# Kernel optimization log

Hardware: AMD Instinct MI355X
Metric: run time of the kernel (lower is better)

The kernel has to match this reference:

```python
import jax, jax.numpy as jnp
import numpy as np

D_MODEL, D_STATE, D_CONV, EXPAND, DEPTH = 128, 16, 4, 2, 4
D_INNER = EXPAND * D_MODEL            # 256
DT_RANK = (D_MODEL + 15) // 16        # 8
C_IN, B, L = 3, 8, 8192


def _layernorm(x, w, b):
    mu = jnp.mean(x, axis=-1, keepdims=True)
    var = jnp.mean((x - mu) ** 2, axis=-1, keepdims=True)
    return (x - mu) * jax.lax.rsqrt(var + 1e-5) * w + b


def _mamba(x, in_w, conv_w, conv_b, xproj_w, dt_w, dt_b, A_log, Dp, out_w):
    # x: [B, L, d_model]
    Bb, Ll, _ = x.shape
    xz = x @ in_w.T                                  # [B,L,2*d_inner]
    u, z = jnp.split(xz, 2, axis=-1)
    # causal depthwise conv1d, kernel D_CONV
    xp = jnp.pad(u, ((0, 0), (D_CONV - 1, 0), (0, 0)))
    conv = conv_b + sum(xp[:, k:k + Ll, :] * conv_w[:, k] for k in range(D_CONV))
    u = jax.nn.silu(conv)                            # [B,L,d_inner]
    dbl = u @ xproj_w.T                              # [B,L,dt_rank+2*d_state]
    dt, Bm, Cm = jnp.split(dbl, [DT_RANK, DT_RANK + D_STATE], axis=-1)
    dt = jax.nn.softplus(dt @ dt_w.T + dt_b)         # [B,L,d_inner]
    A = -jnp.exp(A_log)                              # [d_inner,d_state]

    def step(h, inp):
        dt_t, B_t, C_t, u_t = inp                    # [B,d_inner],[B,d_state],[B,d_state],[B,d_inner]
        dA = jnp.exp(dt_t[..., None] * A)            # [B,d_inner,d_state]
        h = h * dA + (dt_t * u_t)[..., None] * B_t[:, None, :]
        y = jnp.einsum('bds,bs->bd', h, C_t)
        return h, y

    h0 = jnp.zeros((Bb, D_INNER, D_STATE), x.dtype)
    xs = (dt.transpose(1, 0, 2), Bm.transpose(1, 0, 2),
          Cm.transpose(1, 0, 2), u.transpose(1, 0, 2))
    _, ys = jax.lax.scan(step, h0, xs)               # ys: [L,B,d_inner]
    y = ys.transpose(1, 0, 2) + u * Dp
    y = y * jax.nn.silu(z)
    return y @ out_w.T                               # [B,L,d_model]


def setup_inputs() -> dict:
    key = jax.random.key(0)
    ks = jax.random.split(key, 12)
    s = lambda k, shape, scale: jax.random.normal(k, shape, jnp.float32) * scale
    inp = {
        'x': jax.random.normal(ks[0], (B, C_IN, L), jnp.float32),
        'proj_w': s(ks[1], (D_MODEL, C_IN), 0.5),
        'proj_b': jnp.zeros((D_MODEL,), jnp.float32),
        'ln_w': jnp.ones((DEPTH, D_MODEL), jnp.float32),
        'ln_b': jnp.zeros((DEPTH, D_MODEL), jnp.float32),
        'in_w': s(ks[2], (DEPTH, 2 * D_INNER, D_MODEL), D_MODEL ** -0.5),
        'conv_w': s(ks[3], (DEPTH, D_INNER, D_CONV), D_CONV ** -0.5),
        'conv_b': jnp.zeros((DEPTH, D_INNER), jnp.float32),
        'xproj_w': s(ks[4], (DEPTH, DT_RANK + 2 * D_STATE, D_INNER), D_INNER ** -0.5),
        'dt_w': s(ks[5], (DEPTH, D_INNER, DT_RANK), DT_RANK ** -0.5),
        'dt_b': jnp.full((DEPTH, D_INNER), -4.6, jnp.float32),  # softplus ~ small dt
        'A_log': jnp.broadcast_to(jnp.log(jnp.arange(1, D_STATE + 1, dtype=jnp.float32)),
                                  (DEPTH, D_INNER, D_STATE)).copy(),
        'Dp': jnp.ones((DEPTH, D_INNER), jnp.float32),
        'out_w': s(ks[6], (DEPTH, D_MODEL, D_INNER), D_INNER ** -0.5),
        'lnout_w': jnp.ones((D_MODEL,), jnp.float32),
        'lnout_b': jnp.zeros((D_MODEL,), jnp.float32),
    }
    return inp


def reference(x, proj_w, proj_b, ln_w, ln_b, in_w, conv_w, conv_b, xproj_w,
              dt_w, dt_b, A_log, Dp, out_w, lnout_w, lnout_b):
    # proj_in: Conv1d kernel_size=1 == pointwise linear over channels
    h = jnp.einsum('bcl,dc->bld', x, proj_w) + proj_b   # [B,L,d_model]
    for i in range(DEPTH):
        h = h + _mamba(_layernorm(h, ln_w[i], ln_b[i]),
                       in_w[i], conv_w[i], conv_b[i], xproj_w[i],
                       dt_w[i], dt_b[i], A_log[i], Dp[i], out_w[i])
    h = _layernorm(h, lnout_w, lnout_b)
    h_global = h.mean(axis=1)
    return h, h_global
```

## Files before the change

### kernel.cpp

```cpp
#include <hip/hip_runtime.h>
#include <hip/hip_bf16.h>
#include <math.h>

#define Bz     8
#define Lz     8192
#define DM     128
#define DI     256
#define DS     16
#define DTR    8
#define NDBL   40
#define DEPTHN 4
#define BLz    (Bz*Lz)
#define CHT    64
#define NCH    (Lz/CHT)
#define PADI   264
#define PADD   44

typedef unsigned short bf16_t;
typedef __attribute__((ext_vector_type(8))) __bf16 bf8;
typedef __attribute__((ext_vector_type(4))) float f4;
typedef __attribute__((ext_vector_type(8))) unsigned short us8;

__device__ __forceinline__ float bf2f(bf16_t u) {
    return __uint_as_float(((unsigned)u) << 16);
}
__device__ __forceinline__ bf16_t f2bf(float f) {
    unsigned u = __float_as_uint(f);
    u = u + 0x7FFFu + ((u >> 16) & 1u);
    return (bf16_t)(u >> 16);
}
__device__ __forceinline__ float fast_rcp(float x) {
    return __builtin_amdgcn_rcpf(x);
}

__device__ __forceinline__ void pow_tree(float e1, float dA[DS]) {
    float e2 = e1 * e1, e3 = e2 * e1, e4 = e2 * e2;
    float e8 = e4 * e4;
    dA[0] = e1;       dA[1] = e2;       dA[2] = e3;       dA[3] = e4;
    dA[4] = e4 * e1;  dA[5] = e4 * e2;  dA[6] = e4 * e3;  dA[7] = e8;
    dA[8] = e8 * e1;  dA[9] = e8 * e2;  dA[10] = e8 * e3; dA[11] = e8 * e4;
    dA[12] = e8 * dA[4]; dA[13] = e8 * dA[5]; dA[14] = e8 * dA[6];
    dA[15] = e8 * e8;
}

__global__ __launch_bounds__(256) void k_wconv(const float* __restrict__ inw,
                                               const float* __restrict__ ow,
                                               const float* __restrict__ xw,
                                               bf16_t* __restrict__ inwb,
                                               bf16_t* __restrict__ owb,
                                               bf16_t* __restrict__ xwb,
                                               float* __restrict__ hg) {
    int i = blockIdx.x * 256 + threadIdx.x;
    if (i < Bz * DM) hg[i] = 0.f;
    if (i < DEPTHN * 512 * DM) inwb[i] = f2bf(inw[i]);
    if (i < DEPTHN * DM * DI)  owb[i]  = f2bf(ow[i]);
    if (i < DEPTHN * 64 * DI) {
        int layer = i >> 14, rk = i & 16383, r = rk >> 8, k = rk & 255;
        xwb[i] = (r < NDBL) ? f2bf(xw[((size_t)layer * NDBL + r) * DI + k]) : (bf16_t)0;
    }
}

__global__ __launch_bounds__(256) void k_inproj(const float* __restrict__ x,
                                                const float* __restrict__ pw,
                                                const float* __restrict__ pb,
                                                float* __restrict__ h) {
    int t = blockIdx.x * 2 + (threadIdx.x >> 7);
    int d = threadIdx.x & 127;
    int b = t >> 13, l = t & (Lz - 1);
    float acc = pb[d];
#pragma unroll
    for (int c = 0; c < 3; ++c)
        acc += x[(size_t)(b * 3 + c) * Lz + l] * pw[d * 3 + c];
    h[(size_t)t * DM + d] = acc;
}

__global__ __launch_bounds__(256) void k_lnin(const float* __restrict__ h,
                                              const float* __restrict__ lw,
                                              const float* __restrict__ lb,
                                              const bf16_t* __restrict__ inwb,
                                              bf16_t* __restrict__ u_pre,
                                              bf16_t* __restrict__ zs) {
    __shared__ bf16_t sm[64 * PADI];
    bf16_t* xs = sm;
    int tid = threadIdx.x;
    int mBase = blockIdx.x * 64;

#pragma unroll
    for (int p = 0; p < 4; ++p) {
        int row = p * 16 + (tid >> 4);
        int lane = tid & 15;
        const float4* hp = (const float4*)(h + (size_t)(mBase + row) * DM + lane * 8);
        float4 v0 = hp[0], v1 = hp[1];
        float s = v0.x + v0.y + v0.z + v0.w + v1.x + v1.y + v1.z + v1.w;
        float q = v0.x*v0.x + v0.y*v0.y + v0.z*v0.z + v0.w*v0.w +
                  v1.x*v1.x + v1.y*v1.y + v1.z*v1.z + v1.w*v1.w;
#pragma unroll
        for (int off = 1; off < 16; off <<= 1) {
            s += __shfl_xor(s, off);
            q += __shfl_xor(q, off);
        }
        float mean = s * (1.f / DM);
        float var  = q * (1.f / DM) - mean * mean;
        float rstd = rsqrtf(var + 1e-5f);
        const float4* wp = (const float4*)(lw + lane * 8);
        const float4* bp = (const float4*)(lb + lane * 8);
        float4 w0 = wp[0], w1 = wp[1], b0 = bp[0], b1 = bp[1];
        ushort4 o0, o1;
        o0.x = f2bf((v0.x - mean) * rstd * w0.x + b0.x);
        o0.y = f2bf((v0.y - mean) * rstd * w0.y + b0.y);
        o0.z = f2bf((v0.z - mean) * rstd * w0.z + b0.z);
        o0.w = f2bf((v0.w - mean) * rstd * w0.w + b0.w);
        o1.x = f2bf((v1.x - mean) * rstd * w1.x + b1.x);
        o1.y = f2bf((v1.y - mean) * rstd * w1.y + b1.y);
        o1.z = f2bf((v1.z - mean) * rstd * w1.z + b1.z);
        o1.w = f2bf((v1.w - mean) * rstd * w1.w + b1.w);
        *(ushort4*)&xs[row * 136 + lane * 8]     = o0;
        *(ushort4*)&xs[row * 136 + lane * 8 + 4] = o1;
    }
    __syncthreads();

    int wave = tid >> 6, lane = tid & 63;
    int lr = lane & 15, lq = lane >> 4;
    int wn = wave * 128;
    f4 zf = {0.f, 0.f, 0.f, 0.f};
    f4 acc[4][8];
#pragma unroll
    for (int mi = 0; mi < 4; ++mi)
#pragma unroll
        for (int ni = 0; ni < 8; ++ni) acc[mi][ni] = zf;
    const bf16_t* Bp = inwb + (size_t)(wn + lr) * DM + lq * 8;
#pragma unroll
    for (int kk = 0; kk < DM; kk += 32) {
        bf8 af[4], bq[8];
#pragma unroll
        for (int mi = 0; mi < 4; ++mi)
            af[mi] = *(const bf8*)&xs[(mi * 16 + lr) * 136 + lq * 8 + kk];
#pragma unroll
        for (int ni = 0; ni < 8; ++ni)
            bq[ni] = *(const bf8*)(Bp + (size_t)ni * 16 * DM + kk);
#pragma unroll
        for (int mi = 0; mi < 4; ++mi)
#pragma unroll
            for (int ni = 0; ni < 8; ++ni)
                acc[mi][ni] = __builtin_amdgcn_mfma_f32_16x16x32_bf16(
                    af[mi], bq[ni], acc[mi][ni], 0, 0, 0);
    }
    __syncthreads();

    if (wave < 2) {
#pragma unroll
        for (int mi = 0; mi < 4; ++mi)
#pragma unroll
            for (int ni = 0; ni < 8; ++ni)
#pragma unroll
                for (int r = 0; r < 4; ++r)
                    sm[(mi * 16 + lq * 4 + r) * PADI + wn + ni * 16 + lr] =
                        f2bf(acc[mi][ni][r]);
    }
    __syncthreads();
    for (int i = tid; i < 2048; i += 256) {
        int row = i >> 5, col = (i & 31) * 8;
        us8 v = *(const us8*)&sm[row * PADI + col];
        *(us8*)&u_pre[(size_t)(mBase + row) * DI + col] = v;
    }
    __syncthreads();
    if (wave >= 2) {
#pragma unroll
        for (int mi = 0; mi < 4; ++mi)
#pragma unroll
            for (int ni = 0; ni < 8; ++ni)
#pragma unroll
                for (int r = 0; r < 4; ++r) {
                    float v = acc[mi][ni][r];
                    float sil = v * fast_rcp(1.f + __expf(-v));
                    sm[(mi * 16 + lq * 4 + r) * PADI + (wn - 256) + ni * 16 + lr] =
                        f2bf(sil);
                }
    }
    __syncthreads();
    for (int i = tid; i < 2048; i += 256) {
        int row = i >> 5, col = (i & 31) * 8;
        us8 v = *(const us8*)&sm[row * PADI + col];
        *(us8*)&zs[(size_t)(mBase + row) * DI + col] = v;
    }
}

__global__ __launch_bounds__(256, 3) void k_xp_scan1(
        const bf16_t* __restrict__ u_pre, const bf16_t* __restrict__ xwb,
        const float* __restrict__ cw, const float* __restrict__ cb,
        const float* __restrict__ dtw, const float* __restrict__ dtb,
        const float* __restrict__ Alog, const float* __restrict__ Dpv,
        float* __restrict__ dtc, float* __restrict__ Q,
        float* __restrict__ sdtb, bf16_t* __restrict__ ybase) {
    __shared__ bf16_t As[CHT * PADI];
    __shared__ float  Db[CHT * PADD];
    int tid = threadIdx.x;
    size_t tokBase = (size_t)blockIdx.x * CHT;
    int b  = (int)(tokBase >> 13);
    int p0 = (int)(tokBase & (Lz - 1));
    int c  = p0 >> 6;

    int d = tid;
    float hx3 = 0.f, hx2 = 0.f, hx1 = 0.f;
    if (p0 != 0) {
        size_t hb = tokBase * DI + d;
        hx3 = bf2f(u_pre[hb - 3 * DI]);
        hx2 = bf2f(u_pre[hb - 2 * DI]);
        hx1 = bf2f(u_pre[hb - 1 * DI]);
    }
    for (int i = tid; i < 2048; i += 256) {
        int row = i >> 5, col = (i & 31) * 8;
        us8 v = *(const us8*)&u_pre[(tokBase + row) * DI + col];
        *(us8*)&As[row * PADI + col] = v;
    }
    __syncthreads();

    {
        float w0 = cw[d*4+0], w1 = cw[d*4+1], w2 = cw[d*4+2], w3 = cw[d*4+3];
        float bb = cb[d];
        float x3 = hx3, x2 = hx2, x1 = hx1;
#pragma unroll 8
        for (int t = 0; t < CHT; ++t) {
            float x0 = bf2f(As[t * PADI + d]);
            float conv = bb + w0*x3 + w1*x2 + w2*x1 + w3*x0;
            float sil = conv * fast_rcp(1.f + __expf(-conv));
            As[t * PADI + d] = f2bf(sil);
            x3 = x2; x2 = x1; x1 = x0;
        }
    }
    __syncthreads();

    {
        int wave = tid >> 6, lane = tid & 63;
        int lr = lane & 15, lq = lane >> 4;
        int wm = wave * 16;
        f4 zf = {0.f, 0.f, 0.f, 0.f};
        f4 acc[4];
#pragma unroll
        for (int ni = 0; ni < 4; ++ni) acc[ni] = zf;
        const bf16_t* Bp = xwb + (size_t)lr * DI + lq * 8;
#pragma unroll
        for (int kk = 0; kk < DI; kk += 32) {
            bf8 af = *(const bf8*)&As[(wm + lr) * PADI + lq * 8 + kk];
            bf8 bq[4];
#pragma unroll
            for (int ni = 0; ni < 4; ++ni)
                bq[ni] = *(const bf8*)(Bp + (size_t)ni * 16 * DI + kk);
#pragma unroll
            for (int ni = 0; ni < 4; ++ni)
                acc[ni] = __builtin_amdgcn_mfma_f32_16x16x32_bf16(
                    af, bq[ni], acc[ni], 0, 0, 0);
        }
#pragma unroll
        for (int ni = 0; ni < 4; ++ni)
#pragma unroll
            for (int r = 0; r < 4; ++r) {
                int col = ni * 16 + lr;
                if (col < NDBL)
                    Db[(wm + lq * 4 + r) * PADD + col] = acc[ni][r];
            }
    }
    __syncthreads();
    for (int i = tid; i < CHT * 24; i += 256) {
        int row = i / 24, cc = i - row * 24;
        dtc[(tokBase + row) * 24 + cc] = Db[row * PADD + (cc < 8 ? cc : cc + 16)];
    }

    {
        float w[DTR];
#pragma unroll
        for (int r = 0; r < DTR; ++r) w[r] = dtw[d * DTR + r];
        float bb = dtb[d];
        float dp = Dpv[d];
        float a[DS], q[DS];
        const float4* ap = (const float4*)(Alog + d * DS);
#pragma unroll
        for (int s4 = 0; s4 < 4; ++s4) {
            float4 av = ap[s4];
            a[s4*4+0] = -__expf(av.x); a[s4*4+1] = -__expf(av.y);
            a[s4*4+2] = -__expf(av.z); a[s4*4+3] = -__expf(av.w);
        }
#pragma unroll
        for (int s = 0; s < DS; ++s) q[s] = 0.f;
        float a0 = a[0];
        bool fast = true;
#pragma unroll
        for (int s = 1; s < DS; ++s) {
            float ref = a0 * (float)(s + 1);
            fast = fast && (fabsf(a[s] - ref) <= 1e-5f * fabsf(ref) + 1e-7f);
        }
        float sdt = 0.f;
        bf16_t* yp = ybase + tokBase * DI + d;
        if (fast) {
#pragma unroll 4
            for (int t = 0; t < CHT; ++t) {
                float4 r0 = *(const float4*)&Db[t * PADD + 0];
                float4 r1 = *(const float4*)&Db[t * PADD + 4];
                float xv = bb + r0.x*w[0] + r0.y*w[1] + r0.z*w[2] + r0.w*w[3]
                              + r1.x*w[4] + r1.y*w[5] + r1.z*w[6] + r1.w*w[7];
                float dtv = (xv > 20.f) ? xv : __logf(1.f + __expf(xv));
                sdt += dtv;
                float uv = bf2f(As[t * PADI + d]);
                float dtu = dtv * uv;
                float e1 = __expf(dtv * a0);
                float dA[DS];
                pow_tree(e1, dA);
                float bv[DS], cv[DS];
                *(float4*)&bv[0]  = *(const float4*)&Db[t * PADD + 8];
                *(float4*)&bv[4]  = *(const float4*)&Db[t * PADD + 12];
                *(float4*)&bv[8]  = *(const float4*)&Db[t * PADD + 16];
                *(float4*)&bv[12] = *(const float4*)&Db[t * PADD + 20];
                *(float4*)&cv[0]  = *(const float4*)&Db[t * PADD + 24];
                *(float4*)&cv[4]  = *(const float4*)&Db[t * PADD + 28];
                *(float4*)&cv[8]  = *(const float4*)&Db[t * PADD + 32];
                *(float4*)&cv[12] = *(const float4*)&Db[t * PADD + 36];
                float y0 = 0.f, y1 = 0.f, y2 = 0.f, y3 = 0.f;
#pragma unroll
                for (int s = 0; s < DS; s += 4) {
                    q[s]   = q[s]   * dA[s]   + dtu * bv[s];
                    q[s+1] = q[s+1] * dA[s+1] + dtu * bv[s+1];
                    q[s+2] = q[s+2] * dA[s+2] + dtu * bv[s+2];
                    q[s+3] = q[s+3] * dA[s+3] + dtu * bv[s+3];
                    y0 += q[s]   * cv[s];
                    y1 += q[s+1] * cv[s+1];
                    y2 += q[s+2] * cv[s+2];
                    y3 += q[s+3] * cv[s+3];
                }
                float y = (y0 + y1) + (y2 + y3);
                yp[(size_t)t * DI] = f2bf(y + uv * dp);
            }
        } else {
            for (int t = 0; t < CHT; ++t) {
                float4 r0 = *(const float4*)&Db[t * PADD + 0];
                float4 r1 = *(const float4*)&Db[t * PADD + 4];
                float xv = bb + r0.x*w[0] + r0.y*w[1] + r0.z*w[2] + r0.w*w[3]
                              + r1.x*w[4] + r1.y*w[5] + r1.z*w[6] + r1.w*w[7];
                float dtv = (xv > 20.f) ? xv : __logf(1.f + __expf(xv));
                sdt += dtv;
                float uv = bf2f(As[t * PADI + d]);
                float dtu = dtv * uv;
                float bv[DS], cv[DS];
                *(float4*)&bv[0]  = *(const float4*)&Db[t * PADD + 8];
                *(float4*)&bv[4]  = *(const float4*)&Db[t * PADD + 12];
                *(float4*)&bv[8]  = *(const float4*)&Db[t * PADD + 16];
                *(float4*)&bv[12] = *(const float4*)&Db[t * PADD + 20];
                *(float4*)&cv[0]  = *(const float4*)&Db[t * PADD + 24];
                *(float4*)&cv[4]  = *(const float4*)&Db[t * PADD + 28];
                *(float4*)&cv[8]  = *(const float4*)&Db[t * PADD + 32];
                *(float4*)&cv[12] = *(const float4*)&Db[t * PADD + 36];
                float y = 0.f;
#pragma unroll
                for (int s = 0; s < DS; ++s) {
                    float dA = __expf(dtv * a[s]);
                    q[s] = q[s] * dA + dtu * bv[s];
                    y += q[s] * cv[s];
                }
                yp[(size_t)t * DI] = f2bf(y + uv * dp);
            }
        }
        size_t o = ((size_t)(b * NCH + c) * DI + d) * DS;
#pragma unroll
        for (int s = 0; s < DS; s += 4)
            *(float4*)&Q[o + s] = make_float4(q[s], q[s+1], q[s+2], q[s+3]);
        sdtb[(size_t)(b * NCH + c) * DI + d] = sdt;
    }
}

__global__ __launch_bounds__(256) void k_scan2(float* __restrict__ Q,
                                               const float* __restrict__ sdtb,
                                               const float* __restrict__ Alog) {
    int gid = blockIdx.x * 256 + threadIdx.x;
    int b = gid >> 12, r = gid & 4095;
    int d = r >> 4, s = r & 15;
    float a = -__expf(Alog[d * DS + s]);
    const size_t stride = (size_t)DI * DS;
    size_t base = (size_t)b * NCH * stride + r;
    const float* sp = sdtb + (size_t)b * NCH * DI + d;
    float hh = 0.f;
    for (int g = 0; g < NCH / 16; ++g) {
        float qq[16], ee[16];
#pragma unroll
        for (int j = 0; j < 16; ++j)
            qq[j] = Q[base + (size_t)(g * 16 + j) * stride];
#pragma unroll
        for (int j = 0; j < 16; ++j)
            ee[j] = __expf(a * sp[(size_t)(g * 16 + j) * DI]);
#pragma unroll
        for (int j = 0; j < 16; ++j) {
            size_t o = base + (size_t)(g * 16 + j) * stride;
            Q[o] = hh;
            hh = ee[j] * hh + qq[j];
        }
    }
}

__global__ __launch_bounds__(256, 4) void k_corr_out(
        const float* __restrict__ dtc, const bf16_t* __restrict__ ybase,
        const bf16_t* __restrict__ zs,
        const float* __restrict__ dtw, const float* __restrict__ dtb,
        const float* __restrict__ Alog, const float* __restrict__ H0,
        const bf16_t* __restrict__ owb, float* __restrict__ h) {
    __shared__ float epit[CHT * 132];
    __shared__ float Dt8[CHT * 8];
    __shared__ float Cs[CHT * DS];
    bf16_t* yt = (bf16_t*)epit;

    int tid = threadIdx.x;
    size_t tokBase = (size_t)blockIdx.x * CHT;
    int b  = (int)(tokBase >> 13);
    int p0 = (int)(tokBase & (Lz - 1));
    int c  = p0 >> 6;

    for (int i = tid; i < CHT * 24; i += 256) {
        float v = dtc[tokBase * 24 + i];
        int t = i / 24, col = i - t * 24;
        if (col < 8) Dt8[t * 8 + col] = v;
        else         Cs[t * DS + (col - 8)] = v;
    }
    __syncthreads();

    {
        int d = tid;
        float w[DTR];
#pragma unroll
        for (int r = 0; r < DTR; ++r) w[r] = dtw[d * DTR + r];
        float bb = dtb[d];
        float a[DS], gh[DS];
        const float4* ap = (const float4*)(Alog + d * DS);
#pragma unroll
        for (int s4 = 0; s4 < 4; ++s4) {
            float4 av = ap[s4];
            a[s4*4+0] = -__expf(av.x); a[s4*4+1] = -__expf(av.y);
            a[s4*4+2] = -__expf(av.z); a[s4*4+3] = -__expf(av.w);
        }
        size_t ho = ((size_t)(b * NCH + c) * DI + d) * DS;
#pragma unroll
        for (int s = 0; s < DS; s += 4) {
            float4 hv = *(const float4*)&H0[ho + s];
            gh[s] = hv.x; gh[s+1] = hv.y; gh[s+2] = hv.z; gh[s+3] = hv.w;
        }
        float a0 = a[0];
        bool fast = true;
#pragma unroll
        for (int s = 1; s < DS; ++s) {
            float ref = a0 * (float)(s + 1);
            fast = fast && (fabsf(a[s] - ref) <= 1e-5f * fabsf(ref) + 1e-7f);
        }
        const bf16_t* yp = ybase + tokBase * DI + d;
        const bf16_t* zp = zs + tokBase * DI + d;
        float cdt = 0.f;
        float yc[4], zc[4];
#pragma unroll
        for (int j = 0; j < 4; ++j) {
            yc[j] = bf2f(yp[(size_t)j * DI]);
            zc[j] = bf2f(zp[(size_t)j * DI]);
        }
        for (int g = 0; g < CHT / 4; ++g) {
            float yn[4] = {0,0,0,0}, zn[4] = {0,0,0,0};
            if (g + 1 < CHT / 4) {
#pragma unroll
                for (int j = 0; j < 4; ++j) {
                    yn[j] = bf2f(yp[(size_t)((g + 1) * 4 + j) * DI]);
                    zn[j] = bf2f(zp[(size_t)((g + 1) * 4 + j) * DI]);
                }
            }
#pragma unroll
            for (int j = 0; j < 4; ++j) {
                int t = g * 4 + j;
                float4 r0 = *(const float4*)&Dt8[t * 8];
                float4 r1 = *(const float4*)&Dt8[t * 8 + 4];
                float xv = bb + r0.x*w[0] + r0.y*w[1] + r0.z*w[2] + r0.w*w[3]
                              + r1.x*w[4] + r1.y*w[5] + r1.z*w[6] + r1.w*w[7];
                float dtv = (xv > 20.f) ? xv : __logf(1.f + __expf(xv));
                cdt += dtv;
                float cv[DS];
                *(float4*)&cv[0]  = *(const float4*)&Cs[t * DS + 0];
                *(float4*)&cv[4]  = *(const float4*)&Cs[t * DS + 4];
                *(float4*)&cv[8]  = *(const float4*)&Cs[t * DS + 8];
                *(float4*)&cv[12] = *(const float4*)&Cs[t * DS + 12];
                float corr0 = 0.f, corr1 = 0.f, corr2 = 0.f, corr3 = 0.f;
                if (fast) {
                    float e1 = __expf(a0 * cdt);
                    float dA[DS];
                    pow_tree(e1, dA);
#pragma unroll
                    for (int s = 0; s < DS; s += 4) {
                        corr0 += cv[s]   * (gh[s]   * dA[s]);
                        corr1 += cv[s+1] * (gh[s+1] * dA[s+1]);
                        corr2 += cv[s+2] * (gh[s+2] * dA[s+2]);
                        corr3 += cv[s+3] * (gh[s+3] * dA[s+3]);
                    }
                } else {
#pragma unroll
                    for (int s = 0; s < DS; ++s)
                        corr0 += cv[s] * (gh[s] * __expf(a[s] * cdt));
                }
                float y = yc[j] + ((corr0 + corr1) + (corr2 + corr3));
                yt[t * PADI + d] = f2bf(y * zc[j]);
            }
#pragma unroll
            for (int j = 0; j < 4; ++j) { yc[j] = yn[j]; zc[j] = zn[j]; }
        }
    }
    __syncthreads();

    int wave = tid >> 6, lane = tid & 63;
    int lr = lane & 15, lq = lane >> 4;
    int wm = wave * 16;
    f4 zf = {0.f, 0.f, 0.f, 0.f};
    f4 acc[8];
#pragma unroll
    for (int ni = 0; ni < 8; ++ni) acc[ni] = zf;
    const bf16_t* Bp = owb + (size_t)lr * DI + lq * 8;
#pragma unroll
    for (int kk = 0; kk < DI; kk += 32) {
        bf8 af = *(const bf8*)&yt[(wm + lr) * PADI + lq * 8 + kk];
        bf8 bq[8];
#pragma unroll
        for (int ni = 0; ni < 8; ++ni)
            bq[ni] = *(const bf8*)(Bp + (size_t)ni * 16 * DI + kk);
#pragma unroll
        for (int ni = 0; ni < 8; ++ni)
            acc[ni] = __builtin_amdgcn_mfma_f32_16x16x32_bf16(
                af, bq[ni], acc[ni], 0, 0, 0);
    }
    __syncthreads();
#pragma unroll
    for (int ni = 0; ni < 8; ++ni)
#pragma unroll
        for (int r = 0; r < 4; ++r)
            epit[(wm + lq * 4 + r) * 132 + ni * 16 + lr] = acc[ni][r];
    __syncthreads();
    for (int i = tid; i < 2048; i += 256) {
        int row = i >> 5, col = (i & 31) * 4;
        float4 v = *(const float4*)&epit[row * 132 + col];
        float4 old = *(const float4*)&h[(tokBase + row) * DM + col];
        old.x += v.x; old.y += v.y; old.z += v.z; old.w += v.w;
        *(float4*)&h[(tokBase + row) * DM + col] = old;
    }
}

__global__ __launch_bounds__(256) void k_final(float* __restrict__ h,
                                               const float* __restrict__ w,
                                               const float* __restrict__ bias,
                                               float* __restrict__ hg) {
    __shared__ float sbuf[DM];
    int t    = blockIdx.x * 16 + (threadIdx.x >> 4);
    int lane = threadIdx.x & 15;
    int b    = t >> 13;
    if (threadIdx.x < DM) sbuf[threadIdx.x] = 0.f;
    __syncthreads();
    float4* hp = (float4*)(h + (size_t)t * DM + lane * 8);
    float4 v0 = hp[0], v1 = hp[1];
    float s = v0.x + v0.y + v0.z + v0.w + v1.x + v1.y + v1.z + v1.w;
    float q = v0.x*v0.x + v0.y*v0.y + v0.z*v0.z + v0.w*v0.w +
              v1.x*v1.x + v1.y*v1.y + v1.z*v1.z + v1.w*v1.w;
#pragma unroll
    for (int off = 1; off < 16; off <<= 1) {
        s += __shfl_xor(s, off);
        q += __shfl_xor(q, off);
    }
    float mean = s * (1.f / DM);
    float var  = q * (1.f / DM) - mean * mean;
    float rstd = rsqrtf(var + 1e-5f);
    const float4* wp = (const float4*)(w + lane * 8);
    const float4* bp = (const float4*)(bias + lane * 8);
    float4 w0 = wp[0], w1 = wp[1], b0 = bp[0], b1 = bp[1];
    float4 o0, o1;
    o0.x = (v0.x - mean) * rstd * w0.x + b0.x;
    o0.y = (v0.y - mean) * rstd * w0.y + b0.y;
    o0.z = (v0.z - mean) * rstd * w0.z + b0.z;
    o0.w = (v0.w - mean) * rstd * w0.w + b0.w;
    o1.x = (v1.x - mean) * rstd * w1.x + b1.x;
    o1.y = (v1.y - mean) * rstd * w1.y + b1.y;
    o1.z = (v1.z - mean) * rstd * w1.z + b1.z;
    o1.w = (v1.w - mean) * rstd * w1.w + b1.w;
    hp[0] = o0; hp[1] = o1;
    int dbase = lane * 8;
    atomicAdd(&sbuf[dbase + 0], o0.x); atomicAdd(&sbuf[dbase + 1], o0.y);
    atomicAdd(&sbuf[dbase + 2], o0.z); atomicAdd(&sbuf[dbase + 3], o0.w);
    atomicAdd(&sbuf[dbase + 4], o1.x); atomicAdd(&sbuf[dbase + 5], o1.y);
    atomicAdd(&sbuf[dbase + 6], o1.z); atomicAdd(&sbuf[dbase + 7], o1.w);
    __syncthreads();
    if (threadIdx.x < DM)
        atomicAdd(&hg[b * DM + threadIdx.x], sbuf[threadIdx.x] * (1.f / Lz));
}

extern "C" void kernel_launch(void* const* d_in, const int* in_sizes, int n_in,
                              void* d_out, int out_size, void* d_ws, size_t ws_size,
                              hipStream_t stream) {
    const float* x       = (const float*)d_in[0];
    const float* proj_w  = (const float*)d_in[1];
    const float* proj_b  = (const float*)d_in[2];
    const float* ln_w    = (const float*)d_in[3];
    const float* ln_b    = (const float*)d_in[4];
    const float* in_w    = (const float*)d_in[5];
    const float* conv_w  = (const float*)d_in[6];
    const float* conv_b  = (const float*)d_in[7];
    const float* xproj_w = (const float*)d_in[8];
    const float* dt_w    = (const float*)d_in[9];
    const float* dt_b    = (const float*)d_in[10];
    const float* A_log   = (const float*)d_in[11];
    const float* Dp      = (const float*)d_in[12];
    const float* out_w   = (const float*)d_in[13];
    const float* lnout_w = (const float*)d_in[14];
    const float* lnout_b = (const float*)d_in[15];

    float* out = (float*)d_out;
    float* h   = out;
    float* hg  = out + (size_t)BLz * DM;

    char* ws = (char*)d_ws;
    bf16_t* u_pre = (bf16_t*)(ws);
    bf16_t* zs    = (bf16_t*)(ws + 33554432ULL);
    bf16_t* ybase = (bf16_t*)(ws + 67108864ULL);
    float*  dtc   = (float*) (ws + 100663296ULL);
    float*  Q     = (float*) (ws + 106954752ULL);
    float*  sdtb  = (float*) (ws + 123731968ULL);
    bf16_t* inwb  = (bf16_t*)(ws + 124780544ULL);
    bf16_t* owb   = (bf16_t*)(ws + 125304832ULL);
    bf16_t* xwb   = (bf16_t*)(ws + 125566976ULL);

    k_wconv<<<1024, 256, 0, stream>>>(in_w, out_w, xproj_w, inwb, owb, xwb, hg);
    k_inproj<<<BLz / 2, 256, 0, stream>>>(x, proj_w, proj_b, h);

    for (int i = 0; i < DEPTHN; ++i) {
        k_lnin<<<BLz / 64, 256, 0, stream>>>(
            h, ln_w + i * DM, ln_b + i * DM,
            inwb + (size_t)i * 512 * DM, u_pre, zs);
        k_xp_scan1<<<BLz / CHT, 256, 0, stream>>>(
            u_pre, xwb + (size_t)i * 64 * DI,
            conv_w + i * DI * 4, conv_b + i * DI,
            dt_w + i * DI * DTR, dt_b + i * DI, A_log + i * DI * DS,
            Dp + i * DI, dtc, Q, sdtb, ybase);
        k_scan2<<<(Bz * DI * DS) / 256, 256, 0, stream>>>(
            Q, sdtb, A_log + i * DI * DS);
        k_corr_out<<<BLz / CHT, 256, 0, stream>>>(
            dtc, ybase, zs,
            dt_w + i * DI * DTR, dt_b + i * DI,
            A_log + i * DI * DS, Q,
            owb + (size_t)i * DM * DI, h);
    }

    k_final<<<BLz / 16, 256, 0, stream>>>(h, lnout_w, lnout_b, hg);
}
```

Measured before the change: 996.9 us.

## Split scan1 chunk into two halves and shrink scan2 blocks

```diff
diff --git a/kernel.cpp b/kernel.cpp
--- a/kernel.cpp
+++ b/kernel.cpp
@@ -185,7 +185,7 @@
     }
 }
 
-__global__ __launch_bounds__(256, 3) void k_xp_scan1(
+__global__ __launch_bounds__(256, 4) void k_xp_scan1(
         const bf16_t* __restrict__ u_pre, const bf16_t* __restrict__ xwb,
         const float* __restrict__ cw, const float* __restrict__ cb,
         const float* __restrict__ dtw, const float* __restrict__ dtb,
@@ -193,14 +193,14 @@
         float* __restrict__ dtc, float* __restrict__ Q,
         float* __restrict__ sdtb, bf16_t* __restrict__ ybase) {
     __shared__ bf16_t As[CHT * PADI];
-    __shared__ float  Db[CHT * PADD];
+    __shared__ float  Db[32 * PADD];
     int tid = threadIdx.x;
     size_t tokBase = (size_t)blockIdx.x * CHT;
     int b  = (int)(tokBase >> 13);
     int p0 = (int)(tokBase & (Lz - 1));
     int c  = p0 >> 6;
-
-    int d = tid;
+    int d  = tid;
+
     float hx3 = 0.f, hx2 = 0.f, hx1 = 0.f;
     if (p0 != 0) {
         size_t hb = tokBase * DI + d;
@@ -215,92 +215,102 @@
     }
     __syncthreads();
 
+    float cw0 = cw[d*4+0], cw1 = cw[d*4+1], cw2 = cw[d*4+2], cw3 = cw[d*4+3];
+    float cbb = cb[d];
+    float x3 = hx3, x2 = hx2, x1 = hx1;
+#pragma unroll 8
+    for (int t = 0; t < 32; ++t) {
+        float x0 = bf2f(As[t * PADI + d]);
+        float conv = cbb + cw0*x3 + cw1*x2 + cw2*x1 + cw3*x0;
+        float sil = conv * fast_rcp(1.f + __expf(-conv));
+        As[t * PADI + d] = f2bf(sil);
+        x3 = x2; x2 = x1; x1 = x0;
+    }
+    __syncthreads();
+
+    float w[DTR];
+#pragma unroll
+    for (int r = 0; r < DTR; ++r) w[r] = dtw[d * DTR + r];
+    float bb = dtb[d];
+    float dp = Dpv[d];
+    float a0;
+    bool fast;
     {
-        float w0 = cw[d*4+0], w1 = cw[d*4+1], w2 = cw[d*4+2], w3 = cw[d*4+3];
-        float bb = cb[d];
-        float x3 = hx3, x2 = hx2, x1 = hx1;
-#pragma unroll 8
-        for (int t = 0; t < CHT; ++t) {
-            float x0 = bf2f(As[t * PADI + d]);
-            float conv = bb + w0*x3 + w1*x2 + w2*x1 + w3*x0;
-            float sil = conv * fast_rcp(1.f + __expf(-conv));
-            As[t * PADI + d] = f2bf(sil);
-            x3 = x2; x2 = x1; x1 = x0;
-        }
-    }
-    __syncthreads();
-
-    {
-        int wave = tid >> 6, lane = tid & 63;
-        int lr = lane & 15, lq = lane >> 4;
-        int wm = wave * 16;
-        f4 zf = {0.f, 0.f, 0.f, 0.f};
-        f4 acc[4];
-#pragma unroll
-        for (int ni = 0; ni < 4; ++ni) acc[ni] = zf;
-        const bf16_t* Bp = xwb + (size_t)lr * DI + lq * 8;
-#pragma unroll
-        for (int kk = 0; kk < DI; kk += 32) {
-            bf8 af = *(const bf8*)&As[(wm + lr) * PADI + lq * 8 + kk];
-            bf8 bq[4];
-#pragma unroll
-            for (int ni = 0; ni < 4; ++ni)
-                bq[ni] = *(const bf8*)(Bp + (size_t)ni * 16 * DI + kk);
-#pragma unroll
-            for (int ni = 0; ni < 4; ++ni)
-                acc[ni] = __builtin_amdgcn_mfma_f32_16x16x32_bf16(
-                    af, bq[ni], acc[ni], 0, 0, 0);
-        }
-#pragma unroll
-        for (int ni = 0; ni < 4; ++ni)
-#pragma unroll
-            for (int r = 0; r < 4; ++r) {
-                int col = ni * 16 + lr;
-                if (col < NDBL)
-                    Db[(wm + lq * 4 + r) * PADD + col] = acc[ni][r];
-            }
-    }
-    __syncthreads();
-    for (int i = tid; i < CHT * 24; i += 256) {
-        int row = i / 24, cc = i - row * 24;
-        dtc[(tokBase + row) * 24 + cc] = Db[row * PADD + (cc < 8 ? cc : cc + 16)];
-    }
-
-    {
-        float w[DTR];
-#pragma unroll
-        for (int r = 0; r < DTR; ++r) w[r] = dtw[d * DTR + r];
-        float bb = dtb[d];
-        float dp = Dpv[d];
-        float a[DS], q[DS];
+        float aa[DS];
         const float4* ap = (const float4*)(Alog + d * DS);
 #pragma unroll
         for (int s4 = 0; s4 < 4; ++s4) {
             float4 av = ap[s4];
-            a[s4*4+0] = -__expf(av.x); a[s4*4+1] = -__expf(av.y);
-            a[s4*4+2] = -__expf(av.z); a[s4*4+3] = -__expf(av.w);
-        }
-#pragma unroll
-        for (int s = 0; s < DS; ++s) q[s] = 0.f;
-        float a0 = a[0];
-        bool fast = true;
+            aa[s4*4+0] = -__expf(av.x); aa[s4*4+1] = -__expf(av.y);
+            aa[s4*4+2] = -__expf(av.z); aa[s4*4+3] = -__expf(av.w);
+        }
+        a0 = aa[0];
+        fast = true;
 #pragma unroll
         for (int s = 1; s < DS; ++s) {
             float ref = a0 * (float)(s + 1);
-            fast = fast && (fabsf(a[s] - ref) <= 1e-5f * fabsf(ref) + 1e-7f);
-        }
-        float sdt = 0.f;
-        bf16_t* yp = ybase + tokBase * DI + d;
+            fast = fast && (fabsf(aa[s] - ref) <= 1e-5f * fabsf(ref) + 1e-7f);
+        }
+    }
+    float q[DS];
+#pragma unroll
+    for (int s = 0; s < DS; ++s) q[s] = 0.f;
+    float sdt = 0.f;
+
+    int wave = tid >> 6, lane = tid & 63;
+    int lr = lane & 15, lq = lane >> 4;
+    int mt = (wave & 1) * 16;
+    int np = (wave >> 1) * 32;
+    const bf16_t* Bpx = xwb + (size_t)(np + lr) * DI + lq * 8;
+
+    auto do_half = [&](int rbase, bool convB) {
+        {
+            f4 zf = {0.f, 0.f, 0.f, 0.f};
+            f4 acc0 = zf, acc1 = zf;
+#pragma unroll
+            for (int kk = 0; kk < DI; kk += 32) {
+                bf8 af = *(const bf8*)&As[(rbase + mt + lr) * PADI + lq * 8 + kk];
+                bf8 b0 = *(const bf8*)(Bpx + kk);
+                bf8 b1 = *(const bf8*)(Bpx + (size_t)16 * DI + kk);
+                acc0 = __builtin_amdgcn_mfma_f32_16x16x32_bf16(af, b0, acc0, 0, 0, 0);
+                acc1 = __builtin_amdgcn_mfma_f32_16x16x32_bf16(af, b1, acc1, 0, 0, 0);
+            }
+#pragma unroll
+            for (int r = 0; r < 4; ++r) {
+                int row = mt + lq * 4 + r;
+                int c0 = np + lr;
+                if (c0 < NDBL) Db[row * PADD + c0] = acc0[r];
+                int c1 = np + 16 + lr;
+                if (c1 < NDBL) Db[row * PADD + c1] = acc1[r];
+            }
+        }
+        __syncthreads();
+        for (int i = tid; i < 32 * 24; i += 256) {
+            int row = i / 24, cc = i - row * 24;
+            dtc[(tokBase + rbase + row) * 24 + cc] =
+                Db[row * PADD + (cc < 8 ? cc : cc + 16)];
+        }
+        if (convB) {
+#pragma unroll 8
+            for (int t = 32; t < 64; ++t) {
+                float x0 = bf2f(As[t * PADI + d]);
+                float conv = cbb + cw0*x3 + cw1*x2 + cw2*x1 + cw3*x0;
+                float sil = conv * fast_rcp(1.f + __expf(-conv));
+                As[t * PADI + d] = f2bf(sil);
+                x3 = x2; x2 = x1; x1 = x0;
+            }
+        }
+        bf16_t* yp = ybase + (tokBase + rbase) * DI + d;
         if (fast) {
 #pragma unroll 4
-            for (int t = 0; t < CHT; ++t) {
+            for (int t = 0; t < 32; ++t) {
                 float4 r0 = *(const float4*)&Db[t * PADD + 0];
                 float4 r1 = *(const float4*)&Db[t * PADD + 4];
                 float xv = bb + r0.x*w[0] + r0.y*w[1] + r0.z*w[2] + r0.w*w[3]
                               + r1.x*w[4] + r1.y*w[5] + r1.z*w[6] + r1.w*w[7];
                 float dtv = (xv > 20.f) ? xv : __logf(1.f + __expf(xv));
                 sdt += dtv;
-                float uv = bf2f(As[t * PADI + d]);
+                float uv = bf2f(As[(rbase + t) * PADI + d]);
                 float dtu = dtv * uv;
                 float e1 = __expf(dtv * a0);
                 float dA[DS];
@@ -330,14 +340,22 @@
                 yp[(size_t)t * DI] = f2bf(y + uv * dp);
             }
         } else {
-            for (int t = 0; t < CHT; ++t) {
+            float av[DS];
+            const float4* ap = (const float4*)(Alog + d * DS);
+#pragma unroll
+            for (int s4 = 0; s4 < 4; ++s4) {
+                float4 avv = ap[s4];
+                av[s4*4+0] = -__expf(avv.x); av[s4*4+1] = -__expf(avv.y);
+                av[s4*4+2] = -__expf(avv.z); av[s4*4+3] = -__expf(avv.w);
+            }
+            for (int t = 0; t < 32; ++t) {
                 float4 r0 = *(const float4*)&Db[t * PADD + 0];
                 float4 r1 = *(const float4*)&Db[t * PADD + 4];
                 float xv = bb + r0.x*w[0] + r0.y*w[1] + r0.z*w[2] + r0.w*w[3]
                               + r1.x*w[4] + r1.y*w[5] + r1.z*w[6] + r1.w*w[7];
                 float dtv = (xv > 20.f) ? xv : __logf(1.f + __expf(xv));
                 sdt += dtv;
-                float uv = bf2f(As[t * PADI + d]);
+                float uv = bf2f(As[(rbase + t) * PADI + d]);
                 float dtu = dtv * uv;
                 float bv[DS], cv[DS];
                 *(float4*)&bv[0]  = *(const float4*)&Db[t * PADD + 8];
@@ -351,25 +369,29 @@
                 float y = 0.f;
 #pragma unroll
                 for (int s = 0; s < DS; ++s) {
-                    float dA = __expf(dtv * a[s]);
-                    q[s] = q[s] * dA + dtu * bv[s];
+                    float dAv = __expf(dtv * av[s]);
+                    q[s] = q[s] * dAv + dtu * bv[s];
                     y += q[s] * cv[s];
                 }
                 yp[(size_t)t * DI] = f2bf(y + uv * dp);
             }
         }
-        size_t o = ((size_t)(b * NCH + c) * DI + d) * DS;
-#pragma unroll
-        for (int s = 0; s < DS; s += 4)
-            *(float4*)&Q[o + s] = make_float4(q[s], q[s+1], q[s+2], q[s+3]);
-        sdtb[(size_t)(b * NCH + c) * DI + d] = sdt;
-    }
-}
-
-__global__ __launch_bounds__(256) void k_scan2(float* __restrict__ Q,
+        __syncthreads();
+    };
+    do_half(0, true);
+    do_half(32, false);
+
+    size_t o = ((size_t)(b * NCH + c) * DI + d) * DS;
+#pragma unroll
+    for (int s = 0; s < DS; s += 4)
+        *(float4*)&Q[o + s] = make_float4(q[s], q[s+1], q[s+2], q[s+3]);
+    sdtb[(size_t)(b * NCH + c) * DI + d] = sdt;
+}
+
+__global__ __launch_bounds__(128) void k_scan2(float* __restrict__ Q,
                                                const float* __restrict__ sdtb,
                                                const float* __restrict__ Alog) {
-    int gid = blockIdx.x * 256 + threadIdx.x;
+    int gid = blockIdx.x * 128 + threadIdx.x;
     int b = gid >> 12, r = gid & 4095;
     int d = r >> 4, s = r & 15;
     float a = -__expf(Alog[d * DS + s]);
@@ -633,7 +655,7 @@
             conv_w + i * DI * 4, conv_b + i * DI,
             dt_w + i * DI * DTR, dt_b + i * DI, A_log + i * DI * DS,
             Dp + i * DI, dtc, Q, sdtb, ybase);
-        k_scan2<<<(Bz * DI * DS) / 256, 256, 0, stream>>>(
+        k_scan2<<<(Bz * DI * DS) / 128, 128, 0, stream>>>(
             Q, sdtb, A_log + i * DI * DS);
         k_corr_out<<<BLz / CHT, 256, 0, stream>>>(
             dtc, ybase, zs,
```

New measurement: 1.033 ms. +3.6%, slower.

## Fuse layernorm+in-projection into the chunked scan kernel, recomputing conv halo rows

Applied to the files above, without the earlier changes.

```diff
diff --git a/kernel.cpp b/kernel.cpp
--- a/kernel.cpp
+++ b/kernel.cpp
@@ -74,22 +74,42 @@
     h[(size_t)t * DM + d] = acc;
 }
 
-__global__ __launch_bounds__(256) void k_lnin(const float* __restrict__ h,
-                                              const float* __restrict__ lw,
-                                              const float* __restrict__ lb,
-                                              const bf16_t* __restrict__ inwb,
-                                              bf16_t* __restrict__ u_pre,
-                                              bf16_t* __restrict__ zs) {
-    __shared__ bf16_t sm[64 * PADI];
-    bf16_t* xs = sm;
+__global__ __launch_bounds__(256, 3) void k_lnscan(
+        const float* __restrict__ h,
+        const float* __restrict__ lw, const float* __restrict__ lb,
+        const bf16_t* __restrict__ inwb, const bf16_t* __restrict__ xwb,
+        const float* __restrict__ cw, const float* __restrict__ cb,
+        const float* __restrict__ dtw, const float* __restrict__ dtb,
+        const float* __restrict__ Alog, const float* __restrict__ Dpv,
+        bf16_t* __restrict__ zs, float* __restrict__ dtc,
+        float* __restrict__ Q, float* __restrict__ sdtb,
+        bf16_t* __restrict__ ybase) {
+    __shared__ bf16_t As[CHT * PADI];
+    __shared__ char   Rb[18496];
+    bf16_t* xs = (bf16_t*)Rb;
+    bf16_t* zt = (bf16_t*)Rb;
+    float*  Db = (float*)Rb;
+
     int tid = threadIdx.x;
-    int mBase = blockIdx.x * 64;
-
-#pragma unroll
-    for (int p = 0; p < 4; ++p) {
+    size_t tokBase = (size_t)blockIdx.x * CHT;
+    int b  = (int)(tokBase >> 13);
+    int p0 = (int)(tokBase & (Lz - 1));
+    int c  = p0 >> 6;
+    int d  = tid;
+
+#pragma unroll
+    for (int p = 0; p < 5; ++p) {
         int row = p * 16 + (tid >> 4);
+        if (row >= 67) continue;
         int lane = tid & 15;
-        const float4* hp = (const float4*)(h + (size_t)(mBase + row) * DM + lane * 8);
+        if (row >= 64 && p0 == 0) {
+            ushort4 z4 = {0, 0, 0, 0};
+            *(ushort4*)&xs[row * 136 + lane * 8]     = z4;
+            *(ushort4*)&xs[row * 136 + lane * 8 + 4] = z4;
+            continue;
+        }
+        size_t tok = (row < 64) ? (tokBase + row) : (tokBase - 3 + (row - 64));
+        const float4* hp = (const float4*)(h + tok * DM + lane * 8);
         float4 v0 = hp[0], v1 = hp[1];
         float s = v0.x + v0.y + v0.z + v0.w + v1.x + v1.y + v1.z + v1.w;
         float q = v0.x*v0.x + v0.y*v0.y + v0.z*v0.z + v0.w*v0.w +
@@ -121,29 +141,91 @@
 
     int wave = tid >> 6, lane = tid & 63;
     int lr = lane & 15, lq = lane >> 4;
-    int wn = wave * 128;
     f4 zf = {0.f, 0.f, 0.f, 0.f};
-    f4 acc[4][8];
-#pragma unroll
-    for (int mi = 0; mi < 4; ++mi)
-#pragma unroll
-        for (int ni = 0; ni < 8; ++ni) acc[mi][ni] = zf;
-    const bf16_t* Bp = inwb + (size_t)(wn + lr) * DM + lq * 8;
-#pragma unroll
-    for (int kk = 0; kk < DM; kk += 32) {
-        bf8 af[4], bq[8];
+
+    float uh3 = 0.f, uh2 = 0.f, uh1 = 0.f;
+    {
+        int wn = wave * 64;
+        f4 accu[4][4];
+        f4 accH[4];
 #pragma unroll
         for (int mi = 0; mi < 4; ++mi)
-            af[mi] = *(const bf8*)&xs[(mi * 16 + lr) * 136 + lq * 8 + kk];
-#pragma unroll
-        for (int ni = 0; ni < 8; ++ni)
-            bq[ni] = *(const bf8*)(Bp + (size_t)ni * 16 * DM + kk);
+#pragma unroll
+            for (int ni = 0; ni < 4; ++ni) accu[mi][ni] = zf;
+#pragma unroll
+        for (int ni = 0; ni < 4; ++ni) accH[ni] = zf;
+        const bf16_t* Bp = inwb + (size_t)(wn + lr) * DM + lq * 8;
+#pragma unroll
+        for (int kk = 0; kk < DM; kk += 32) {
+            bf8 af[4], afh, bq[4];
+#pragma unroll
+            for (int mi = 0; mi < 4; ++mi)
+                af[mi] = *(const bf8*)&xs[(mi * 16 + lr) * 136 + lq * 8 + kk];
+            afh = *(const bf8*)&xs[(51 + lr) * 136 + lq * 8 + kk];
+#pragma unroll
+            for (int ni = 0; ni < 4; ++ni)
+                bq[ni] = *(const bf8*)(Bp + (size_t)ni * 16 * DM + kk);
+#pragma unroll
+            for (int mi = 0; mi < 4; ++mi)
+#pragma unroll
+                for (int ni = 0; ni < 4; ++ni)
+                    accu[mi][ni] = __builtin_amdgcn_mfma_f32_16x16x32_bf16(
+                        af[mi], bq[ni], accu[mi][ni], 0, 0, 0);
+#pragma unroll
+            for (int ni = 0; ni < 4; ++ni)
+                accH[ni] = __builtin_amdgcn_mfma_f32_16x16x32_bf16(
+                    afh, bq[ni], accH[ni], 0, 0, 0);
+        }
 #pragma unroll
         for (int mi = 0; mi < 4; ++mi)
 #pragma unroll
-            for (int ni = 0; ni < 8; ++ni)
-                acc[mi][ni] = __builtin_amdgcn_mfma_f32_16x16x32_bf16(
-                    af[mi], bq[ni], acc[mi][ni], 0, 0, 0);
+            for (int ni = 0; ni < 4; ++ni)
+#pragma unroll
+                for (int r = 0; r < 4; ++r)
+                    As[(mi * 16 + lq * 4 + r) * PADI + wn + ni * 16 + lr] =
+                        f2bf(accu[mi][ni][r]);
+
+        if (p0 != 0) {
+            int src   = 48 + (d & 15);
+            int nisel = (d >> 4) & 3;
+            float hv[3];
+#pragma unroll
+            for (int j = 0; j < 3; ++j) {
+                float v0 = __shfl(bf2f(f2bf(accH[0][j + 1])), src);
+                float v1 = __shfl(bf2f(f2bf(accH[1][j + 1])), src);
+                float v2 = __shfl(bf2f(f2bf(accH[2][j + 1])), src);
+                float v3 = __shfl(bf2f(f2bf(accH[3][j + 1])), src);
+                hv[j] = (nisel == 0) ? v0 : (nisel == 1) ? v1
+                      : (nisel == 2) ? v2 : v3;
+            }
+            uh3 = hv[0]; uh2 = hv[1]; uh1 = hv[2];
+        }
+    }
+
+    f4 accz[4][4];
+    {
+        int wnz = 256 + wave * 64;
+#pragma unroll
+        for (int mi = 0; mi < 4; ++mi)
+#pragma unroll
+            for (int ni = 0; ni < 4; ++ni) accz[mi][ni] = zf;
+        const bf16_t* Bp = inwb + (size_t)(wnz + lr) * DM + lq * 8;
+#pragma unroll
+        for (int kk = 0; kk < DM; kk += 32) {
+            bf8 af[4], bq[4];
+#pragma unroll
+            for (int mi = 0; mi < 4; ++mi)
+                af[mi] = *(const bf8*)&xs[(mi * 16 + lr) * 136 + lq * 8 + kk];
+#pragma unroll
+            for (int ni = 0; ni < 4; ++ni)
+                bq[ni] = *(const bf8*)(Bp + (size_t)ni * 16 * DM + kk);
+#pragma unroll
+            for (int mi = 0; mi < 4; ++mi)
+#pragma unroll
+                for (int ni = 0; ni < 4; ++ni)
+                    accz[mi][ni] = __builtin_amdgcn_mfma_f32_16x16x32_bf16(
+                        af[mi], bq[ni], accz[mi][ni], 0, 0, 0);
+        }
     }
     __syncthreads();
 
@@ -151,78 +233,51 @@
 #pragma unroll
         for (int mi = 0; mi < 4; ++mi)
 #pragma unroll
-            for (int ni = 0; ni < 8; ++ni)
-#pragma unroll
-                for (int r = 0; r < 4; ++r)
-                    sm[(mi * 16 + lq * 4 + r) * PADI + wn + ni * 16 + lr] =
-                        f2bf(acc[mi][ni][r]);
-    }
-    __syncthreads();
-    for (int i = tid; i < 2048; i += 256) {
-        int row = i >> 5, col = (i & 31) * 8;
-        us8 v = *(const us8*)&sm[row * PADI + col];
-        *(us8*)&u_pre[(size_t)(mBase + row) * DI + col] = v;
-    }
-    __syncthreads();
-    if (wave >= 2) {
-#pragma unroll
-        for (int mi = 0; mi < 4; ++mi)
-#pragma unroll
-            for (int ni = 0; ni < 8; ++ni)
+            for (int ni = 0; ni < 4; ++ni)
 #pragma unroll
                 for (int r = 0; r < 4; ++r) {
-                    float v = acc[mi][ni][r];
+                    float v = accz[mi][ni][r];
                     float sil = v * fast_rcp(1.f + __expf(-v));
-                    sm[(mi * 16 + lq * 4 + r) * PADI + (wn - 256) + ni * 16 + lr] =
+                    zt[(mi * 16 + lq * 4 + r) * 136 + wave * 64 + ni * 16 + lr] =
                         f2bf(sil);
                 }
     }
     __syncthreads();
-    for (int i = tid; i < 2048; i += 256) {
-        int row = i >> 5, col = (i & 31) * 8;
-        us8 v = *(const us8*)&sm[row * PADI + col];
-        *(us8*)&zs[(size_t)(mBase + row) * DI + col] = v;
-    }
-}
-
-__global__ __launch_bounds__(256, 3) void k_xp_scan1(
-        const bf16_t* __restrict__ u_pre, const bf16_t* __restrict__ xwb,
-        const float* __restrict__ cw, const float* __restrict__ cb,
-        const float* __restrict__ dtw, const float* __restrict__ dtb,
-        const float* __restrict__ Alog, const float* __restrict__ Dpv,
-        float* __restrict__ dtc, float* __restrict__ Q,
-        float* __restrict__ sdtb, bf16_t* __restrict__ ybase) {
-    __shared__ bf16_t As[CHT * PADI];
-    __shared__ float  Db[CHT * PADD];
-    int tid = threadIdx.x;
-    size_t tokBase = (size_t)blockIdx.x * CHT;
-    int b  = (int)(tokBase >> 13);
-    int p0 = (int)(tokBase & (Lz - 1));
-    int c  = p0 >> 6;
-
-    int d = tid;
-    float hx3 = 0.f, hx2 = 0.f, hx1 = 0.f;
-    if (p0 != 0) {
-        size_t hb = tokBase * DI + d;
-        hx3 = bf2f(u_pre[hb - 3 * DI]);
-        hx2 = bf2f(u_pre[hb - 2 * DI]);
-        hx1 = bf2f(u_pre[hb - 1 * DI]);
-    }
-    for (int i = tid; i < 2048; i += 256) {
-        int row = i >> 5, col = (i & 31) * 8;
-        us8 v = *(const us8*)&u_pre[(tokBase + row) * DI + col];
-        *(us8*)&As[row * PADI + col] = v;
+    for (int i = tid; i < 1024; i += 256) {
+        int row = i >> 4, col = (i & 15) * 8;
+        us8 v = *(const us8*)&zt[row * 136 + col];
+        *(us8*)&zs[(tokBase + row) * DI + col] = v;
+    }
+    __syncthreads();
+    if (wave >= 2) {
+#pragma unroll
+        for (int mi = 0; mi < 4; ++mi)
+#pragma unroll
+            for (int ni = 0; ni < 4; ++ni)
+#pragma unroll
+                for (int r = 0; r < 4; ++r) {
+                    float v = accz[mi][ni][r];
+                    float sil = v * fast_rcp(1.f + __expf(-v));
+                    zt[(mi * 16 + lq * 4 + r) * 136 + (wave - 2) * 64 + ni * 16 + lr] =
+                        f2bf(sil);
+                }
+    }
+    __syncthreads();
+    for (int i = tid; i < 1024; i += 256) {
+        int row = i >> 4, col = (i & 15) * 8;
+        us8 v = *(const us8*)&zt[row * 136 + col];
+        *(us8*)&zs[(tokBase + row) * DI + 128 + col] = v;
     }
     __syncthreads();
 
     {
-        float w0 = cw[d*4+0], w1 = cw[d*4+1], w2 = cw[d*4+2], w3 = cw[d*4+3];
-        float bb = cb[d];
-        float x3 = hx3, x2 = hx2, x1 = hx1;
+        float cw0 = cw[d*4+0], cw1 = cw[d*4+1], cw2 = cw[d*4+2], cw3 = cw[d*4+3];
+        float cbb = cb[d];
+        float x3 = uh3, x2 = uh2, x1 = uh1;
 #pragma unroll 8
         for (int t = 0; t < CHT; ++t) {
             float x0 = bf2f(As[t * PADI + d]);
-            float conv = bb + w0*x3 + w1*x2 + w2*x1 + w3*x0;
+            float conv = cbb + cw0*x3 + cw1*x2 + cw2*x1 + cw3*x0;
             float sil = conv * fast_rcp(1.f + __expf(-conv));
             As[t * PADI + d] = f2bf(sil);
             x3 = x2; x2 = x1; x1 = x0;
@@ -231,10 +286,7 @@
     __syncthreads();
 
     {
-        int wave = tid >> 6, lane = tid & 63;
-        int lr = lane & 15, lq = lane >> 4;
         int wm = wave * 16;
-        f4 zf = {0.f, 0.f, 0.f, 0.f};
         f4 acc[4];
 #pragma unroll
         for (int ni = 0; ni < 4; ++ni) acc[ni] = zf;
@@ -366,10 +418,10 @@
     }
 }
 
-__global__ __launch_bounds__(256) void k_scan2(float* __restrict__ Q,
+__global__ __launch_bounds__(128) void k_scan2(float* __restrict__ Q,
                                                const float* __restrict__ sdtb,
                                                const float* __restrict__ Alog) {
-    int gid = blockIdx.x * 256 + threadIdx.x;
+    int gid = blockIdx.x * 128 + threadIdx.x;
     int b = gid >> 12, r = gid & 4095;
     int d = r >> 4, s = r & 15;
     float a = -__expf(Alog[d * DS + s]);
@@ -611,7 +663,6 @@
     float* hg  = out + (size_t)BLz * DM;
 
     char* ws = (char*)d_ws;
-    bf16_t* u_pre = (bf16_t*)(ws);
     bf16_t* zs    = (bf16_t*)(ws + 33554432ULL);
     bf16_t* ybase = (bf16_t*)(ws + 67108864ULL);
     float*  dtc   = (float*) (ws + 100663296ULL);
@@ -625,15 +676,13 @@
     k_inproj<<<BLz / 2, 256, 0, stream>>>(x, proj_w, proj_b, h);
 
     for (int i = 0; i < DEPTHN; ++i) {
-        k_lnin<<<BLz / 64, 256, 0, stream>>>(
+        k_lnscan<<<BLz / CHT, 256, 0, stream>>>(
             h, ln_w + i * DM, ln_b + i * DM,
-            inwb + (size_t)i * 512 * DM, u_pre, zs);
-        k_xp_scan1<<<BLz / CHT, 256, 0, stream>>>(
-            u_pre, xwb + (size_t)i * 64 * DI,
+            inwb + (size_t)i * 512 * DM, xwb + (size_t)i * 64 * DI,
             conv_w + i * DI * 4, conv_b + i * DI,
             dt_w + i * DI * DTR, dt_b + i * DI, A_log + i * DI * DS,
-            Dp + i * DI, dtc, Q, sdtb, ybase);
-        k_scan2<<<(Bz * DI * DS) / 256, 256, 0, stream>>>(
+            Dp + i * DI, zs, dtc, Q, sdtb, ybase);
+        k_scan2<<<(Bz * DI * DS) / 128, 128, 0, stream>>>(
             Q, sdtb, A_log + i * DI * DS);
         k_corr_out<<<BLz / CHT, 256, 0, stream>>>(
             dtc, ybase, zs,
```

Result: faster. 882.2 us (-11.5%).
